# Optimization experiments

Hardware: AMD Instinct MI355X
Metric: run time of the kernel (lower is better)

The kernel has to match this reference:

```python
import jax, jax.numpy as jnp
import numpy as np

BATCH = 8192
IN_FEATURES = 4096
OUT_FEATURES = 4096
PACKED_LEN = (IN_FEATURES + 7) // 8  # 512


def _unpack_pm1(x_packed):
    """Unpack uint8-valued ints (stored as int32) into +/-1 float32, LSB-first.
    [.., P] -> [.., P*8]; bit 1 -> +1.0, bit 0 -> -1.0."""
    bits = (x_packed[..., None] >> jnp.arange(8, dtype=x_packed.dtype)) & 1
    bits = bits.reshape(*x_packed.shape[:-1], x_packed.shape[-1] * 8)
    return (2.0 * bits - 1.0).astype(jnp.float32)


def setup_inputs() -> dict:
    key = jax.random.key(0)
    k1, k2, k3 = jax.random.split(key, 3)
    input_packed = jax.random.randint(k1, (BATCH, PACKED_LEN), 0, 256, dtype=jnp.int32)
    weight_packed = jax.random.randint(k2, (OUT_FEATURES, PACKED_LEN), 0, 256, dtype=jnp.int32)
    bias = jax.random.normal(k3, (OUT_FEATURES,), dtype=jnp.float32) * 0.01
    return {"input_packed": input_packed, "weight_packed": weight_packed, "bias": bias}


def reference(input_packed, weight_packed, bias):
    # BitLinear: +/-1 dot product == in_features - 2*popcount(a XOR w)
    a = _unpack_pm1(input_packed)   # [B, in_features]
    w = _unpack_pm1(weight_packed)  # [out_features, in_features]
    out = jnp.einsum('bk,ok->bo', a, w)  # fp32 accumulate, [B, out_features]
    return out + bias
```

## Files before the change

### kernel.cpp

```cpp
#include <hip/hip_runtime.h>
#include <stdint.h>


typedef int v4i  __attribute__((ext_vector_type(4)));
typedef int v16i __attribute__((ext_vector_type(16)));

#define BATCH 8192
#define OUTF  4096
#define KDIM  4096
#define BM    128
#define BN    256
#define BKB   128

__device__ inline void expand8(uint32_t x, uint32_t& lo, uint32_t& hi) {
    lo = 0u; hi = 0u;
#pragma unroll
    for (int j = 0; j < 4; ++j) {
        lo |= ((((x >> j)       & 1u) * 2u - 1u) & 0xFFu) << (8 * j);
        hi |= ((((x >> (j + 4)) & 1u) * 2u - 1u) & 0xFFu) << (8 * j);
    }
}

__device__ inline void unpack_one(const int* __restrict__ src, int4* __restrict__ dst,
                                  int t) {
    const int r = t & 31;
    const int s = (t >> 5) & 3;
    const int c = (t >> 7) & 31;
    const int g = t >> 12;
    const int m = g * 32 + r;
    int4 v = ((const int4*)src)[m * 128 + c * 4 + s];
    uint32_t l0, h0, l1, h1, l2, h2, l3, h3;
    expand8((uint32_t)v.x, l0, h0);
    expand8((uint32_t)v.y, l1, h1);
    expand8((uint32_t)v.z, l2, h2);
    expand8((uint32_t)v.w, l3, h3);
    const int idx = (g * 32 + c) * 256 + s * 64 + r;
    int4 o0; o0.x = (int)l0; o0.y = (int)h0; o0.z = (int)l1; o0.w = (int)h1;
    int4 o1; o1.x = (int)l2; o1.y = (int)h2; o1.z = (int)l3; o1.w = (int)h3;
    dst[idx]      = o0;
    dst[idx + 32] = o1;
}

__global__ __launch_bounds__(256) void unpack_kernel(const int* __restrict__ a_packed,
                                                     const int* __restrict__ w_packed,
                                                     char* __restrict__ Ai8,
                                                     char* __restrict__ Wi8) {
    const int A_WORK = BATCH * 128;
    const int W_WORK = OUTF * 128;
    int t = blockIdx.x * 256 + threadIdx.x;
    if (t < A_WORK) {
        unpack_one(a_packed, (int4*)Ai8, t);
    } else {
        t -= A_WORK;
        if (t < W_WORK) unpack_one(w_packed, (int4*)Wi8, t);
    }
}

__global__ __launch_bounds__(256, 2) void bitgemm_mfma(const char* __restrict__ A,
                                                       const char* __restrict__ W,
                                                       const float* __restrict__ bias,
                                                       float* __restrict__ out) {
    __shared__ __attribute__((aligned(16))) char lds[48 * 1024];

    const int tid  = threadIdx.x;
    const int lane = tid & 63;
    const int w    = __builtin_amdgcn_readfirstlane(tid >> 6);
    const int m0   = blockIdx.y * BM;
    const int n0   = blockIdx.x * BN;

    const char* pA = A + (size_t)blockIdx.y * 4 * 131072 + lane * 16;
    const char* pW = W + (size_t)blockIdx.x * 8 * 131072 + lane * 16;

    const int mtb = (w & 1) * 2;
    const int ntb = (w >> 1) * 4;

    v16i acc[2][4];
#pragma unroll
    for (int mt = 0; mt < 2; ++mt)
#pragma unroll
        for (int nt = 0; nt < 4; ++nt)
#pragma unroll
            for (int r = 0; r < 16; ++r) acc[mt][nt][r] = 0;

    const v4i* fA = (const v4i*)(lds) + mtb * 4 * 64 + lane;
    const v4i* fW = (const v4i*)(lds + 16 * 1024) + ntb * 4 * 64 + lane;

#pragma unroll 1
    for (int kc = 0; kc < KDIM; kc += BKB) {
#pragma unroll
        for (int j = 0; j < 12; ++j) {
            int bi = w * 12 + j;
            const char* g;
            if (bi < 16) g = pA + (bi >> 2) * 131072 + (bi & 3) * 1024;
            else {
                int b2 = bi - 16;
                g = pW + (b2 >> 2) * 131072 + (b2 & 3) * 1024;
            }
            __builtin_amdgcn_global_load_lds(
                (const __attribute__((address_space(1))) void*)g,
                (__attribute__((address_space(3))) void*)(lds + bi * 1024),
                16, 0, 0);
        }
        __syncthreads();

#pragma unroll
        for (int s = 0; s < 4; ++s) {
            v4i av[2], wv[4];
#pragma unroll
            for (int mt = 0; mt < 2; ++mt) av[mt] = fA[(mt * 4 + s) * 64];
#pragma unroll
            for (int nt = 0; nt < 4; ++nt) wv[nt] = fW[(nt * 4 + s) * 64];
#pragma unroll
            for (int mt = 0; mt < 2; ++mt)
#pragma unroll
                for (int nt = 0; nt < 4; ++nt)
                    acc[mt][nt] = __builtin_amdgcn_mfma_i32_32x32x32_i8(
                        av[mt], wv[nt], acc[mt][nt], 0, 0, 0);
        }
        __syncthreads();
        pA += 4096; pW += 4096;
    }

    const int cl = lane & 31;
    const int r0 = (lane >> 5) * 4;
#pragma unroll
    for (int mt = 0; mt < 2; ++mt) {
        const int rowbase = m0 + (mtb + mt) * 32 + r0;
#pragma unroll
        for (int nt = 0; nt < 4; ++nt) {
            const int col = n0 + (ntb + nt) * 32 + cl;
            const float bv = bias[col];
#pragma unroll
            for (int r = 0; r < 16; ++r) {
                const int row = rowbase + (r & 3) + 8 * (r >> 2);
                out[(size_t)row * OUTF + col] = (float)acc[mt][nt][r] + bv;
            }
        }
    }
}

extern "C" void kernel_launch(void* const* d_in, const int* in_sizes, int n_in,
                              void* d_out, int out_size, void* d_ws, size_t ws_size,
                              hipStream_t stream) {
    const int*   a_packed = (const int*)d_in[0];
    const int*   w_packed = (const int*)d_in[1];
    const float* bias     = (const float*)d_in[2];
    float*       out      = (float*)d_out;

    char* Ai8 = (char*)d_ws;
    char* Wi8 = Ai8 + (size_t)BATCH * KDIM;

    const int total = BATCH * 128 + OUTF * 128;
    unpack_kernel<<<total / 256, 256, 0, stream>>>(a_packed, w_packed, Ai8, Wi8);

    dim3 grid(OUTF / BN, BATCH / BM);
    bitgemm_mfma<<<grid, 256, 0, stream>>>(Ai8, Wi8, bias, out);
}
```

Baseline: 291.4 us.

## Double-buffer LDS in int8 MFMA GEMM with 256x256 tiles and faster unpack

The GEMM tile grows to 256x256 with 512 threads (8 waves, 4x2 MFMA tiles each), and the LDS staging is double-buffered so the next K-chunk's global_load_lds is issued before computing on the current one. The second barrier per iteration goes away, and s_setprio is raised around the MFMA bursts. The unpack kernel now has each thread handle four int4 words and builds the ±1 bytes with multiply/mask bit tricks instead of per-bit loops. The 128KB LDS request and larger register footprint may limit occupancy to one block per CU.

```diff
diff --git a/kernel.cpp b/kernel.cpp
--- a/kernel.cpp
+++ b/kernel.cpp
@@ -8,132 +8,145 @@
 #define BATCH 8192
 #define OUTF  4096
 #define KDIM  4096
-#define BM    128
+#define BM    256
 #define BN    256
 #define BKB   128
+#define NSTEP (KDIM / BKB)
 
-__device__ inline void expand8(uint32_t x, uint32_t& lo, uint32_t& hi) {
-    lo = 0u; hi = 0u;
-#pragma unroll
-    for (int j = 0; j < 4; ++j) {
-        lo |= ((((x >> j)       & 1u) * 2u - 1u) & 0xFFu) << (8 * j);
-        hi |= ((((x >> (j + 4)) & 1u) * 2u - 1u) & 0xFFu) << (8 * j);
-    }
-}
-
-__device__ inline void unpack_one(const int* __restrict__ src, int4* __restrict__ dst,
-                                  int t) {
-    const int r = t & 31;
-    const int s = (t >> 5) & 3;
-    const int c = (t >> 7) & 31;
-    const int g = t >> 12;
-    const int m = g * 32 + r;
-    int4 v = ((const int4*)src)[m * 128 + c * 4 + s];
-    uint32_t l0, h0, l1, h1, l2, h2, l3, h3;
-    expand8((uint32_t)v.x, l0, h0);
-    expand8((uint32_t)v.y, l1, h1);
-    expand8((uint32_t)v.z, l2, h2);
-    expand8((uint32_t)v.w, l3, h3);
-    const int idx = (g * 32 + c) * 256 + s * 64 + r;
-    int4 o0; o0.x = (int)l0; o0.y = (int)h0; o0.z = (int)l1; o0.w = (int)h1;
-    int4 o1; o1.x = (int)l2; o1.y = (int)h2; o1.z = (int)l3; o1.w = (int)h3;
-    dst[idx]      = o0;
-    dst[idx + 32] = o1;
+__device__ __forceinline__ void expand_word(uint32_t x, uint32_t& pl, uint32_t& ph) {
+    uint32_t lo = ((x & 0xFu) * 0x204081u) & 0x01010101u;
+    uint32_t hi = (((x >> 4) & 0xFu) * 0x204081u) & 0x01010101u;
+    pl = ~((lo << 8) - (lo << 1));
+    ph = ~((hi << 8) - (hi << 1));
 }
 
 __global__ __launch_bounds__(256) void unpack_kernel(const int* __restrict__ a_packed,
                                                      const int* __restrict__ w_packed,
                                                      char* __restrict__ Ai8,
                                                      char* __restrict__ Wi8) {
-    const int A_WORK = BATCH * 128;
-    const int W_WORK = OUTF * 128;
+    const int A_WORK = BATCH * 32;
     int t = blockIdx.x * 256 + threadIdx.x;
-    if (t < A_WORK) {
-        unpack_one(a_packed, (int4*)Ai8, t);
-    } else {
-        t -= A_WORK;
-        if (t < W_WORK) unpack_one(w_packed, (int4*)Wi8, t);
+    const int* __restrict__ src = a_packed;
+    int4* dst = (int4*)Ai8;
+    if (t >= A_WORK) { t -= A_WORK; src = w_packed; dst = (int4*)Wi8; }
+
+    const int r = t & 31;
+    const int c = (t >> 5) & 31;
+    const int g = t >> 10;
+    const int m = g * 32 + r;
+
+    const int4* s4 = (const int4*)src + (m * 128 + c * 4);
+    int4 v0 = s4[0], v1 = s4[1], v2 = s4[2], v3 = s4[3];
+
+    int4* dbase = dst + ((g * 32 + c) * 256 + r);
+
+#define EMIT(S, V)                                                     \
+    {                                                                  \
+        uint32_t l0, h0, l1, h1, l2, h2, l3, h3;                       \
+        expand_word((uint32_t)(V).x, l0, h0);                          \
+        expand_word((uint32_t)(V).y, l1, h1);                          \
+        expand_word((uint32_t)(V).z, l2, h2);                          \
+        expand_word((uint32_t)(V).w, l3, h3);                          \
+        int4 o0 = make_int4((int)l0, (int)h0, (int)l1, (int)h1);       \
+        int4 o1 = make_int4((int)l2, (int)h2, (int)l3, (int)h3);       \
+        dbase[(S) * 64]      = o0;                         \
+        dbase[(S) * 64 + 32] = o1;                         \
     }
+    EMIT(0, v0) EMIT(1, v1) EMIT(2, v2) EMIT(3, v3)
+#undef EMIT
 }
 
-__global__ __launch_bounds__(256, 2) void bitgemm_mfma(const char* __restrict__ A,
+__global__ __launch_bounds__(512, 2) void bitgemm_mfma(const char* __restrict__ A,
                                                        const char* __restrict__ W,
                                                        const float* __restrict__ bias,
                                                        float* __restrict__ out) {
-    __shared__ __attribute__((aligned(16))) char lds[48 * 1024];
+    __shared__ __attribute__((aligned(16))) char lds[2 * 65536];
 
     const int tid  = threadIdx.x;
     const int lane = tid & 63;
     const int w    = __builtin_amdgcn_readfirstlane(tid >> 6);
-    const int m0   = blockIdx.y * BM;
-    const int n0   = blockIdx.x * BN;
+    const int wr   = w >> 2;
+    const int wc   = w & 3;
+    const int bx   = blockIdx.x;
+    const int by   = blockIdx.y;
 
-    const char* pA = A + (size_t)blockIdx.y * 4 * 131072 + lane * 16;
-    const char* pW = W + (size_t)blockIdx.x * 8 * 131072 + lane * 16;
+    const char* baseA = A + (size_t)by * 8 * 131072 + (size_t)lane * 16;
+    const char* baseW = W + (size_t)bx * 8 * 131072 + (size_t)lane * 16;
 
-    const int mtb = (w & 1) * 2;
-    const int ntb = (w >> 1) * 4;
+    v16i acc[4][2];
+#pragma unroll
+    for (int mt = 0; mt < 4; ++mt)
+#pragma unroll
+        for (int nt = 0; nt < 2; ++nt)
+#pragma unroll
+            for (int rg = 0; rg < 16; ++rg) acc[mt][nt][rg] = 0;
 
-    v16i acc[2][4];
+    auto stage = [&](int kc, int buf) {
+        char* ldst = lds + buf * 65536;
 #pragma unroll
-    for (int mt = 0; mt < 2; ++mt)
-#pragma unroll
-        for (int nt = 0; nt < 4; ++nt)
-#pragma unroll
-            for (int r = 0; r < 16; ++r) acc[mt][nt][r] = 0;
-
-    const v4i* fA = (const v4i*)(lds) + mtb * 4 * 64 + lane;
-    const v4i* fW = (const v4i*)(lds + 16 * 1024) + ntb * 4 * 64 + lane;
-
-#pragma unroll 1
-    for (int kc = 0; kc < KDIM; kc += BKB) {
-#pragma unroll
-        for (int j = 0; j < 12; ++j) {
-            int bi = w * 12 + j;
+        for (int j = 0; j < 8; ++j) {
+            const int bi = w * 8 + j;
             const char* g;
-            if (bi < 16) g = pA + (bi >> 2) * 131072 + (bi & 3) * 1024;
-            else {
-                int b2 = bi - 16;
-                g = pW + (b2 >> 2) * 131072 + (b2 & 3) * 1024;
+            if (bi < 32) {
+                g = baseA + (bi >> 2) * 131072 + (bi & 3) * 1024 + kc * 4096;
+            } else {
+                const int b2 = bi - 32;
+                g = baseW + (b2 >> 2) * 131072 + (b2 & 3) * 1024 + kc * 4096;
             }
             __builtin_amdgcn_global_load_lds(
                 (const __attribute__((address_space(1))) void*)g,
-                (__attribute__((address_space(3))) void*)(lds + bi * 1024),
+                (__attribute__((address_space(3))) void*)(ldst + bi * 1024),
                 16, 0, 0);
         }
+    };
+
+    const int aoff = wr * 16384 + lane * 16;
+    const int woff = 32768 + wc * 8192 + lane * 16;
+
+    stage(0, 0);
+    int cur = 0;
+#pragma unroll 1
+    for (int kc = 0; kc < NSTEP; ++kc) {
         __syncthreads();
+        if (kc < NSTEP - 1) stage(kc + 1, cur ^ 1);
 
+        const char* ldsC = lds + cur * 65536;
 #pragma unroll
         for (int s = 0; s < 4; ++s) {
-            v4i av[2], wv[4];
+            v4i av[4], wv[2];
 #pragma unroll
-            for (int mt = 0; mt < 2; ++mt) av[mt] = fA[(mt * 4 + s) * 64];
+            for (int mt = 0; mt < 4; ++mt)
+                av[mt] = *(const v4i*)(ldsC + aoff + (mt * 4 + s) * 1024);
 #pragma unroll
-            for (int nt = 0; nt < 4; ++nt) wv[nt] = fW[(nt * 4 + s) * 64];
+            for (int nt = 0; nt < 2; ++nt)
+                wv[nt] = *(const v4i*)(ldsC + woff + (nt * 4 + s) * 1024);
+            __builtin_amdgcn_s_setprio(1);
 #pragma unroll
-            for (int mt = 0; mt < 2; ++mt)
+            for (int mt = 0; mt < 4; ++mt)
 #pragma unroll
-                for (int nt = 0; nt < 4; ++nt)
+                for (int nt = 0; nt < 2; ++nt)
                     acc[mt][nt] = __builtin_amdgcn_mfma_i32_32x32x32_i8(
                         av[mt], wv[nt], acc[mt][nt], 0, 0, 0);
+            __builtin_amdgcn_s_setprio(0);
         }
-        __syncthreads();
-        pA += 4096; pW += 4096;
+        cur ^= 1;
     }
 
     const int cl = lane & 31;
     const int r0 = (lane >> 5) * 4;
+    const int m0 = by * BM;
+    const int n0 = bx * BN;
 #pragma unroll
-    for (int mt = 0; mt < 2; ++mt) {
-        const int rowbase = m0 + (mtb + mt) * 32 + r0;
+    for (int mt = 0; mt < 4; ++mt) {
+        const int rowbase = m0 + (wr * 4 + mt) * 32 + r0;
 #pragma unroll
-        for (int nt = 0; nt < 4; ++nt) {
-            const int col = n0 + (ntb + nt) * 32 + cl;
+        for (int nt = 0; nt < 2; ++nt) {
+            const int col = n0 + (wc * 2 + nt) * 32 + cl;
             const float bv = bias[col];
 #pragma unroll
-            for (int r = 0; r < 16; ++r) {
-                const int row = rowbase + (r & 3) + 8 * (r >> 2);
-                out[(size_t)row * OUTF + col] = (float)acc[mt][nt][r] + bv;
+            for (int rg = 0; rg < 16; ++rg) {
+                const int row = rowbase + (rg & 3) + 8 * (rg >> 2);
+                out[(size_t)row * OUTF + col] = (float)acc[mt][nt][rg] + bv;
             }
         }
     }
@@ -150,9 +163,9 @@
     char* Ai8 = (char*)d_ws;
     char* Wi8 = Ai8 + (size_t)BATCH * KDIM;
 
-    const int total = BATCH * 128 + OUTF * 128;
+    const int total = (BATCH + OUTF) * 32;
     unpack_kernel<<<total / 256, 256, 0, stream>>>(a_packed, w_packed, Ai8, Wi8);
 
     dim3 grid(OUTF / BN, BATCH / BM);
-    bitgemm_mfma<<<grid, 256, 0, stream>>>(Ai8, Wi8, bias, out);
+    bitgemm_mfma<<<grid, 512, 0, stream>>>(Ai8, Wi8, bias, out);
 }
```

After: 259.6 us. -10.9%, faster.
